# Kernel optimization log

Hardware: AMD Instinct MI355X
Metric: run time of the kernel (lower is better)

Reference implementation:

```python
import jax, jax.numpy as jnp
import numpy as np

D_MODEL = 1024
NUM_HEADS = 16
D_K = D_MODEL // NUM_HEADS


def setup_inputs() -> dict:
    key = jax.random.key(0)
    ks = jax.random.split(key, 11)
    B, S = 4, 2048
    s = 1.0 / np.sqrt(D_MODEL)
    return {
        "query": jax.random.normal(ks[0], (B, S, D_MODEL), jnp.float32),
        "key": jax.random.normal(ks[1], (B, S, D_MODEL), jnp.float32),
        "value": jax.random.normal(ks[2], (B, S, D_MODEL), jnp.float32),
        "Wq": jax.random.normal(ks[3], (D_MODEL, D_MODEL), jnp.float32) * s,
        "bq": jnp.zeros((D_MODEL,), jnp.float32),
        "Wk": jax.random.normal(ks[4], (D_MODEL, D_MODEL), jnp.float32) * s,
        "bk": jnp.zeros((D_MODEL,), jnp.float32),
        "Wv": jax.random.normal(ks[5], (D_MODEL, D_MODEL), jnp.float32) * s,
        "bv": jnp.zeros((D_MODEL,), jnp.float32),
        "Wo": jax.random.normal(ks[6], (D_MODEL, D_MODEL), jnp.float32) * s,
        "bo": jnp.zeros((D_MODEL,), jnp.float32),
    }


def reference(query, key, value, Wq, bq, Wk, bk, Wv, bv, Wo, bo):
    B, Sq, _ = query.shape
    Sk = key.shape[1]
    # linear projections (torch Linear: x @ W.T + b)
    q = query @ Wq.T + bq
    k = key @ Wk.T + bk
    v = value @ Wv.T + bv
    # [B, H, S, d_k]
    q = q.reshape(B, Sq, NUM_HEADS, D_K).transpose(0, 2, 1, 3)
    k = k.reshape(B, Sk, NUM_HEADS, D_K).transpose(0, 2, 1, 3)
    v = v.reshape(B, Sk, NUM_HEADS, D_K).transpose(0, 2, 1, 3)
    scores = jnp.einsum("bhqd,bhkd->bhqk", q, k) / jnp.sqrt(jnp.float32(D_K)).astype(q.dtype)
    attn = jax.nn.softmax(scores, axis=-1)
    out = jnp.einsum("bhqk,bhkd->bhqd", attn, v)
    out = out.transpose(0, 2, 1, 3).reshape(B, Sq, D_MODEL)
    return out @ Wo.T + bo
```

## Files before the change

kernel.cpp:

```cpp
#include <hip/hip_runtime.h>
#include <hip/hip_bf16.h>
#include <cstdint>
#include <cstddef>

typedef __attribute__((ext_vector_type(8))) short bf16x8;
typedef __attribute__((ext_vector_type(4))) short bf16x4;
typedef __attribute__((ext_vector_type(4))) float f32x4;
typedef __attribute__((ext_vector_type(2))) unsigned int u32x2;
typedef __attribute__((ext_vector_type(4))) unsigned int u32x4;

#define NH 16
#define DK 64
#define SEQ 2048
#define DM 1024
#define QSCALE 0.18033688011112042f

__device__ __forceinline__ short f2bf(float f) {
    union { float f; unsigned u; } x; x.f = f;
    unsigned r = x.u + 0x7fffu + ((x.u >> 16) & 1u);
    return (short)(r >> 16);
}

__device__ __forceinline__ unsigned pk2(float a, float b) {
    union { float f; unsigned u; } x, y; x.f = a; y.f = b;
    return __builtin_amdgcn_perm(y.u + 0x8000u, x.u + 0x8000u, 0x07060302u);
}

__device__ __forceinline__ unsigned cvtpk(float a, float b) {
    unsigned r;
    asm("v_cvt_pk_bf16_f32 %0, %1, %2" : "=v"(r) : "v"(a), "v"(b));
    return r;
}

__device__ __forceinline__ void plswap32(unsigned& a, unsigned& b) {
    asm("v_permlane32_swap_b32 %0, %1" : "+v"(a), "+v"(b));
}

__device__ __forceinline__ void glds16(const short* g, short* l) {
    __builtin_amdgcn_global_load_lds((const __attribute__((address_space(1))) unsigned int*)g,
                                     (__attribute__((address_space(3))) unsigned int*)l, 16, 0, 0);
}

__global__ __launch_bounds__(256)
void cvt_all(const float* __restrict__ xq, const float* __restrict__ xk, const float* __restrict__ xv,
             const float* __restrict__ Wq, const float* __restrict__ Wk,
             const float* __restrict__ Wv, const float* __restrict__ Wo,
             short* __restrict__ xb0, short* __restrict__ xb1, short* __restrict__ xb2,
             short* __restrict__ Wb)
{
    const int bid = blockIdx.x;
    const float* src;
    short* dst;
    float sc = 1.0f;
    int i;
    if (bid < 12288) {
        int z = bid >> 12;
        src = (z == 0) ? xq : (z == 1) ? xk : xv;
        dst = (z == 0) ? xb0 : (z == 1) ? xb1 : xb2;
        i = (bid & 4095) * 2048 + threadIdx.x * 8;
    } else {
        int wb = bid - 12288;
        int z = wb >> 9;
        src = (z == 0) ? Wq : (z == 1) ? Wk : (z == 2) ? Wv : Wo;
        dst = Wb + (size_t)z * DM * DM;
        sc = (z == 0) ? QSCALE : 1.0f;
        i = (wb & 511) * 2048 + threadIdx.x * 8;
    }
    float4 a = *(const float4*)&src[i];
    float4 b = *(const float4*)&src[i + 4];
    bf16x8 o = { f2bf(a.x * sc), f2bf(a.y * sc), f2bf(a.z * sc), f2bf(a.w * sc),
                 f2bf(b.x * sc), f2bf(b.y * sc), f2bf(b.z * sc), f2bf(b.w * sc) };
    *(bf16x8*)&dst[i] = o;
}

__global__ __launch_bounds__(256)
void cvt_x(const float* __restrict__ src, short* __restrict__ dst)
{
    int i = (blockIdx.x * 256 + threadIdx.x) * 8;
    float4 a = *(const float4*)&src[i];
    float4 b = *(const float4*)&src[i + 4];
    bf16x8 o = { f2bf(a.x), f2bf(a.y), f2bf(a.z), f2bf(a.w),
                 f2bf(b.x), f2bf(b.y), f2bf(b.z), f2bf(b.w) };
    *(bf16x8*)&dst[i] = o;
}

__global__ __launch_bounds__(256)
void cvt_w(const float* __restrict__ Wq, const float* __restrict__ Wk,
           const float* __restrict__ Wv, const float* __restrict__ Wo,
           short* __restrict__ dst)
{
    int z = blockIdx.y;
    const float* s = (z == 0) ? Wq : (z == 1) ? Wk : (z == 2) ? Wv : Wo;
    float sc = (z == 0) ? QSCALE : 1.0f;
    int i = (blockIdx.x * 256 + threadIdx.x) * 8;
    float4 a = *(const float4*)&s[i];
    float4 b = *(const float4*)&s[i + 4];
    bf16x8 o = { f2bf(a.x * sc), f2bf(a.y * sc), f2bf(a.z * sc), f2bf(a.w * sc),
                 f2bf(b.x * sc), f2bf(b.y * sc), f2bf(b.z * sc), f2bf(b.w * sc) };
    *(bf16x8*)&dst[(size_t)z * DM * DM + i] = o;
}

#define GEMM_CORE(P0, OFF0, P1, OFF1)                                                      \
    __shared__ short As[128 * 32];                                                         \
    __shared__ short Bs[128 * 32];                                                         \
    f32x4 acc[4][4] = {};                                                                  \
    const int t = threadIdx.x;                                                             \
    const int lane = t & 63;                                                               \
    const int w = t >> 6;                                                                  \
    const int wm = (w >> 1) * 64, wn = (w & 1) * 64;                                       \
    const int l15 = lane & 15, quad = lane >> 4;                                           \
    const int g0 = t, g1 = 256 + t;                                                        \
    const int r0 = g0 >> 2, r1 = g1 >> 2;                                                  \
    const int c0 = ((g0 & 3) ^ ((r0 >> 1) & 3)) * 8;                                       \
    const int c1 = ((g1 & 3) ^ ((r1 >> 1) & 3)) * 8;                                       \
    for (int k0 = 0; k0 < DM; k0 += 32) {                                                  \
        glds16(&P0[(size_t)(OFF0 + r0) * DM + k0 + c0], &As[g0 * 8]);                      \
        glds16(&P0[(size_t)(OFF0 + r1) * DM + k0 + c1], &As[g1 * 8]);                      \
        glds16(&P1[(size_t)(OFF1 + r0) * DM + k0 + c0], &Bs[g0 * 8]);                      \
        glds16(&P1[(size_t)(OFF1 + r1) * DM + k0 + c1], &Bs[g1 * 8]);                      \
        __syncthreads();                                                                   \
        bf16x8 a[4], b[4];                                                                 \
        _Pragma("unroll")                                                                  \
        for (int i = 0; i < 4; i++) {                                                      \
            int row = wm + i * 16 + l15;                                                   \
            a[i] = *(bf16x8*)&As[row * 32 + (quad ^ ((row >> 1) & 3)) * 8];                \
        }                                                                                  \
        _Pragma("unroll")                                                                  \
        for (int j = 0; j < 4; j++) {                                                      \
            int row = wn + j * 16 + l15;                                                   \
            b[j] = *(bf16x8*)&Bs[row * 32 + (quad ^ ((row >> 1) & 3)) * 8];                \
        }                                                                                  \
        _Pragma("unroll")                                                                  \
        for (int i = 0; i < 4; i++)                                                        \
            _Pragma("unroll")                                                              \
            for (int j = 0; j < 4; j++)                                                    \
                acc[i][j] = __builtin_amdgcn_mfma_f32_16x16x32_bf16(a[i], b[j], acc[i][j], 0, 0, 0); \
        __syncthreads();                                                                   \
    }

__global__ __launch_bounds__(256)
void gemm_qkv(const short* __restrict__ x0, const short* __restrict__ x1, const short* __restrict__ x2,
              const short* __restrict__ Wball,
              const float* __restrict__ bq, const float* __restrict__ bk, const float* __restrict__ bv,
              short* __restrict__ qws, short* __restrict__ kws, short* __restrict__ vws,
              int zoff)
{
    const int z = blockIdx.z + zoff;
    const short* X = (z == 0) ? x0 : (z == 1) ? x1 : x2;
    const short* W = Wball + (size_t)z * DM * DM;
    const float* bias = (z == 0) ? bq : (z == 1) ? bk : bv;
    const float bscale = (z == 0) ? QSCALE : 1.0f;

    const int tn = blockIdx.x * 128;
    const int tm = blockIdx.y * 128;
    const int vm = (z == 2);

    const short* P0 = vm ? X : W;   const int OFF0 = vm ? tm : tn;
    const short* P1 = vm ? W : X;   const int OFF1 = vm ? tn : tm;
    GEMM_CORE(P0, OFF0, P1, OFF1)

    if (vm) {
#pragma unroll
        for (int j = 0; j < 4; j++) {
            int n = tn + wn + j * 16 + l15;
            float bn = bias[n];
            int h = n >> 6, d = n & 63;
#pragma unroll
            for (int i = 0; i < 4; i++) {
                int m0 = tm + wm + i * 16 + quad * 4;
                int bb = m0 >> 11, s0 = m0 & (SEQ - 1);
                int g = (s0 >> 2) & 7;
                int gp = (g & 4) | ((g & 1) << 1) | ((g >> 1) & 1);
                int sp = (s0 & ~31) | (gp << 2);
                u32x2 u = { pk2(acc[i][j][0] + bn, acc[i][j][1] + bn),
                            pk2(acc[i][j][2] + bn, acc[i][j][3] + bn) };
                *(u32x2*)&vws[((size_t)((bb * NH + h) * 64 + d)) * SEQ + sp] = u;
            }
        }
    } else {
        short* dst = (z == 0) ? qws : kws;
#pragma unroll
        for (int i = 0; i < 4; i++) {
            int n0 = tn + wm + i * 16 + quad * 4;
            float4 b4 = *(const float4*)&bias[n0];
            int h = n0 >> 6, d0 = n0 & 63;
#pragma unroll
            for (int j = 0; j < 4; j++) {
                int m = tm + wn + j * 16 + l15;
                int bb = m >> 11, s = m & (SEQ - 1);
                u32x2 u = { pk2(acc[i][j][0] + b4.x * bscale, acc[i][j][1] + b4.y * bscale),
                            pk2(acc[i][j][2] + b4.z * bscale, acc[i][j][3] + b4.w * bscale) };
                *(u32x2*)&dst[((((size_t)(bb * NH + h)) * SEQ + s) << 6) + d0] = u;
            }
        }
    }
}

__global__ __launch_bounds__(256)
void out_proj(const short* __restrict__ A, const short* __restrict__ W,
              const float* __restrict__ bias, float* __restrict__ out)
{
    const int tn = blockIdx.x * 128;
    const int tm = blockIdx.y * 128;
    GEMM_CORE(A, tm, W, tn)

#pragma unroll
    for (int j = 0; j < 4; j++) {
        int n = tn + wn + j * 16 + l15;
        float bn = bias[n];
#pragma unroll
        for (int i = 0; i < 4; i++)
#pragma unroll
            for (int r = 0; r < 4; r++) {
                int m = tm + wm + i * 16 + quad * 4 + r;
                out[(size_t)m * DM + n] = acc[i][j][r] + bn;
            }
    }
}

__global__ __launch_bounds__(256, 4)
void attn(const short* __restrict__ Q, const short* __restrict__ K, const short* __restrict__ V,
          short* __restrict__ O)
{
    const int qt = blockIdx.x;
    const int bh = blockIdx.y;
    const int b = bh >> 4, h = bh & 15;
    const size_t base = (size_t)bh * SEQ * DK;
    const size_t vbase = (size_t)bh * DK * SEQ;

    const int t = threadIdx.x;
    const int lane = t & 63;
    const int w = t >> 6;
    const int l15 = lane & 15, quad = lane >> 4;
    const int l7 = l15 & 7;

    __shared__ short Kt[2][64 * 64];
    __shared__ short Vt[2][80 * 64];

    {
        int buf = t >> 7;
        int row = 64 + ((t >> 3) & 15);
        short val = (row == 64) ? (short)0x3F80 : (short)0;
        bf16x8 fill = { val, val, val, val, val, val, val, val };
        *(bf16x8*)&Vt[buf][row * 64 + (t & 7) * 8] = fill;
    }

    const int sr = t >> 3, su = t & 7;
    const int swz = (su ^ (sr & 7)) * 8;
    const short* kp0 = &K[base + (size_t)sr * DK + swz];
    const short* vp0 = &V[vbase + (size_t)sr * SEQ + swz];

    glds16(kp0,               &Kt[0][sr * 64 + su * 8]);
    glds16(kp0 + 32 * DK,     &Kt[0][(32 + sr) * 64 + su * 8]);
    glds16(vp0,               &Vt[0][sr * 64 + su * 8]);
    glds16(vp0 + 32 * SEQ,    &Vt[0][(32 + sr) * 64 + su * 8]);

    bf16x8 qb[2][2];
    const int qrow0 = qt * 128 + w * 32;
#pragma unroll
    for (int nq = 0; nq < 2; nq++)
#pragma unroll
        for (int kd = 0; kd < 2; kd++)
            qb[nq][kd] = *(const bf16x8*)&Q[base + (size_t)(qrow0 + nq * 16 + l15) * DK + kd * 32 + quad * 8];

    f32x4 oT[5][2] = {};

    for (int kt = 0; kt < SEQ / 64; kt++) {
        __syncthreads();
        const int cur = kt & 1;
        if (kt < SEQ / 64 - 1) {
            const int nxt = cur ^ 1;
            const int kb = (kt + 1) * 64;
            glds16(kp0 + (size_t)kb * DK,        &Kt[nxt][sr * 64 + su * 8]);
            glds16(kp0 + (size_t)(kb + 32) * DK, &Kt[nxt][(32 + sr) * 64 + su * 8]);
            glds16(vp0 + kb,                     &Vt[nxt][sr * 64 + su * 8]);
            glds16(vp0 + kb + 32 * SEQ,          &Vt[nxt][(32 + sr) * 64 + su * 8]);
        }

#pragma unroll
        for (int half = 0; half < 2; half++) {
            f32x4 st[2][2] = {};
#pragma unroll
            for (int kd = 0; kd < 2; kd++) {
#pragma unroll
                for (int m2 = 0; m2 < 2; m2++) {
                    const int mf = half * 2 + m2;
                    bf16x8 ka = *(bf16x8*)&Kt[cur][(mf * 16 + l15) * 64 + ((kd * 4 + quad) ^ l7) * 8];
#pragma unroll
                    for (int nq = 0; nq < 2; nq++)
                        st[m2][nq] = __builtin_amdgcn_mfma_f32_16x16x32_bf16(ka, qb[nq][kd], st[m2][nq], 0, 0, 0);
                }
            }

            bf16x8 pb[2];
#pragma unroll
            for (int nq = 0; nq < 2; nq++) {
#pragma unroll
                for (int m2 = 0; m2 < 2; m2++)
#pragma unroll
                    for (int r = 0; r < 4; r++)
                        st[m2][nq][r] = __builtin_amdgcn_exp2f(st[m2][nq][r]);
                unsigned W0 = cvtpk(st[0][nq][0], st[0][nq][1]);
                unsigned W1 = cvtpk(st[0][nq][2], st[0][nq][3]);
                unsigned W2 = cvtpk(st[1][nq][0], st[1][nq][1]);
                unsigned W3 = cvtpk(st[1][nq][2], st[1][nq][3]);
                plswap32(W0, W2);
                plswap32(W1, W3);
                u32x4 uu = { W0, W1, W2, W3 };
                pb[nq] = *(bf16x8*)&uu;
            }

#pragma unroll
            for (int mfd = 0; mfd < 5; mfd++) {
                bf16x8 va = *(bf16x8*)&Vt[cur][(mfd * 16 + l15) * 64 + ((half * 4 + quad) ^ l7) * 8];
#pragma unroll
                for (int nq = 0; nq < 2; nq++)
                    oT[mfd][nq] = __builtin_amdgcn_mfma_f32_16x16x32_bf16(va, pb[nq], oT[mfd][nq], 0, 0, 0);
            }
        }
    }

#pragma unroll
    for (int nq = 0; nq < 2; nq++) {
        float lsum = __shfl(oT[4][nq][0], l15);
        float inv = 1.0f / lsum;
        int s = qrow0 + nq * 16 + l15;
#pragma unroll
        for (int mfd = 0; mfd < 4; mfd++) {
            u32x2 u = { cvtpk(oT[mfd][nq][0] * inv, oT[mfd][nq][1] * inv),
                        cvtpk(oT[mfd][nq][2] * inv, oT[mfd][nq][3] * inv) };
            *(u32x2*)&O[((size_t)(b * SEQ + s)) * DM + h * 64 + mfd * 16 + quad * 4] = u;
        }
    }
}

extern "C" void kernel_launch(void* const* d_in, const int* in_sizes, int n_in,
                              void* d_out, int out_size, void* d_ws, size_t ws_size,
                              hipStream_t stream)
{
    const float* q_in = (const float*)d_in[0];
    const float* k_in = (const float*)d_in[1];
    const float* v_in = (const float*)d_in[2];
    const float* Wq = (const float*)d_in[3];
    const float* bq = (const float*)d_in[4];
    const float* Wk = (const float*)d_in[5];
    const float* bk = (const float*)d_in[6];
    const float* Wv = (const float*)d_in[7];
    const float* bv = (const float*)d_in[8];
    const float* Wo = (const float*)d_in[9];
    const float* bo = (const float*)d_in[10];
    float* out = (float*)d_out;

    char* ws = (char*)d_ws;
    const size_t MB = (size_t)1024 * 1024;
    short* qws = (short*)d_out;
    short* kws = (short*)d_out + (size_t)8 * MB;
    const size_t NW = (size_t)DM * DM;

    if (ws_size >= 88 * MB) {
        short* xb0 = (short*)(ws);
        short* xb1 = (short*)(ws + 16 * MB);
        short* xb2 = (short*)(ws + 32 * MB);
        short* vws = (short*)(ws + 48 * MB);
        short* ows = (short*)(ws + 64 * MB);
        short* Wb  = (short*)(ws + 80 * MB);

        cvt_all<<<dim3(14336), 256, 0, stream>>>(q_in, k_in, v_in, Wq, Wk, Wv, Wo, xb0, xb1, xb2, Wb);
        gemm_qkv<<<dim3(8, 64, 3), 256, 0, stream>>>(xb0, xb1, xb2, Wb, bq, bk, bv, qws, kws, vws, 0);
        attn<<<dim3(16, 64), 256, 0, stream>>>(qws, kws, vws, ows);
        out_proj<<<dim3(8, 64), 256, 0, stream>>>(ows, Wb + 3 * NW, bo, out);
    } else {
        short* xb  = (short*)(ws);
        short* vws = (short*)(ws + 16 * MB);
        short* ows = (short*)(ws + 32 * MB);
        short* Wb  = (short*)(ws + 48 * MB);
        const int xblocks = (4 * SEQ * DM) / 2048;

        cvt_w<<<dim3((int)(NW / 2048), 4), 256, 0, stream>>>(Wq, Wk, Wv, Wo, Wb);
        cvt_x<<<dim3(xblocks), 256, 0, stream>>>(q_in, xb);
        gemm_qkv<<<dim3(8, 64, 1), 256, 0, stream>>>(xb, xb, xb, Wb, bq, bk, bv, qws, kws, vws, 0);
        cvt_x<<<dim3(xblocks), 256, 0, stream>>>(k_in, xb);
        gemm_qkv<<<dim3(8, 64, 1), 256, 0, stream>>>(xb, xb, xb, Wb, bq, bk, bv, qws, kws, vws, 1);
        cvt_x<<<dim3(xblocks), 256, 0, stream>>>(v_in, xb);
        gemm_qkv<<<dim3(8, 64, 1), 256, 0, stream>>>(xb, xb, xb, Wb, bq, bk, bv, qws, kws, vws, 2);
        attn<<<dim3(16, 64), 256, 0, stream>>>(qws, kws, vws, ows);
        out_proj<<<dim3(8, 64), 256, 0, stream>>>(ows, Wb + 3 * NW, bo, out);
    }
}
```

Before: 345.8 us.

## Double attention query tile per block to reuse K/V tiles across more rows

```diff
diff --git a/kernel.cpp b/kernel.cpp
--- a/kernel.cpp
+++ b/kernel.cpp
@@ -218,7 +218,7 @@
     }
 }
 
-__global__ __launch_bounds__(256, 4)
+__global__ __launch_bounds__(256, 2)
 void attn(const short* __restrict__ Q, const short* __restrict__ K, const short* __restrict__ V,
           short* __restrict__ O)
 {
@@ -255,15 +255,15 @@
     glds16(vp0,               &Vt[0][sr * 64 + su * 8]);
     glds16(vp0 + 32 * SEQ,    &Vt[0][(32 + sr) * 64 + su * 8]);
 
-    bf16x8 qb[2][2];
-    const int qrow0 = qt * 128 + w * 32;
-#pragma unroll
-    for (int nq = 0; nq < 2; nq++)
+    bf16x8 qb[4][2];
+    const int qrow0 = qt * 256 + w * 64;
+#pragma unroll
+    for (int nq = 0; nq < 4; nq++)
 #pragma unroll
         for (int kd = 0; kd < 2; kd++)
             qb[nq][kd] = *(const bf16x8*)&Q[base + (size_t)(qrow0 + nq * 16 + l15) * DK + kd * 32 + quad * 8];
 
-    f32x4 oT[5][2] = {};
+    f32x4 oT[5][4] = {};
 
     for (int kt = 0; kt < SEQ / 64; kt++) {
         __syncthreads();
@@ -279,49 +279,56 @@
 
 #pragma unroll
         for (int half = 0; half < 2; half++) {
-            f32x4 st[2][2] = {};
-#pragma unroll
-            for (int kd = 0; kd < 2; kd++) {
-#pragma unroll
-                for (int m2 = 0; m2 < 2; m2++) {
-                    const int mf = half * 2 + m2;
-                    bf16x8 ka = *(bf16x8*)&Kt[cur][(mf * 16 + l15) * 64 + ((kd * 4 + quad) ^ l7) * 8];
-#pragma unroll
-                    for (int nq = 0; nq < 2; nq++)
-                        st[m2][nq] = __builtin_amdgcn_mfma_f32_16x16x32_bf16(ka, qb[nq][kd], st[m2][nq], 0, 0, 0);
+            bf16x8 ka[2][2];
+#pragma unroll
+            for (int m2 = 0; m2 < 2; m2++)
+#pragma unroll
+                for (int kd = 0; kd < 2; kd++)
+                    ka[m2][kd] = *(bf16x8*)&Kt[cur][((half * 2 + m2) * 16 + l15) * 64 + ((kd * 4 + quad) ^ l7) * 8];
+
+            bf16x8 pb[4];
+#pragma unroll
+            for (int np = 0; np < 2; np++) {
+                f32x4 st[2][2] = {};
+#pragma unroll
+                for (int kd = 0; kd < 2; kd++)
+#pragma unroll
+                    for (int m2 = 0; m2 < 2; m2++)
+#pragma unroll
+                        for (int n2 = 0; n2 < 2; n2++)
+                            st[m2][n2] = __builtin_amdgcn_mfma_f32_16x16x32_bf16(
+                                ka[m2][kd], qb[np * 2 + n2][kd], st[m2][n2], 0, 0, 0);
+
+#pragma unroll
+                for (int n2 = 0; n2 < 2; n2++) {
+#pragma unroll
+                    for (int m2 = 0; m2 < 2; m2++)
+#pragma unroll
+                        for (int r = 0; r < 4; r++)
+                            st[m2][n2][r] = __builtin_amdgcn_exp2f(st[m2][n2][r]);
+                    unsigned W0 = cvtpk(st[0][n2][0], st[0][n2][1]);
+                    unsigned W1 = cvtpk(st[0][n2][2], st[0][n2][3]);
+                    unsigned W2 = cvtpk(st[1][n2][0], st[1][n2][1]);
+                    unsigned W3 = cvtpk(st[1][n2][2], st[1][n2][3]);
+                    plswap32(W0, W2);
+                    plswap32(W1, W3);
+                    u32x4 uu = { W0, W1, W2, W3 };
+                    pb[np * 2 + n2] = *(bf16x8*)&uu;
                 }
-            }
-
-            bf16x8 pb[2];
-#pragma unroll
-            for (int nq = 0; nq < 2; nq++) {
-#pragma unroll
-                for (int m2 = 0; m2 < 2; m2++)
-#pragma unroll
-                    for (int r = 0; r < 4; r++)
-                        st[m2][nq][r] = __builtin_amdgcn_exp2f(st[m2][nq][r]);
-                unsigned W0 = cvtpk(st[0][nq][0], st[0][nq][1]);
-                unsigned W1 = cvtpk(st[0][nq][2], st[0][nq][3]);
-                unsigned W2 = cvtpk(st[1][nq][0], st[1][nq][1]);
-                unsigned W3 = cvtpk(st[1][nq][2], st[1][nq][3]);
-                plswap32(W0, W2);
-                plswap32(W1, W3);
-                u32x4 uu = { W0, W1, W2, W3 };
-                pb[nq] = *(bf16x8*)&uu;
             }
 
 #pragma unroll
             for (int mfd = 0; mfd < 5; mfd++) {
                 bf16x8 va = *(bf16x8*)&Vt[cur][(mfd * 16 + l15) * 64 + ((half * 4 + quad) ^ l7) * 8];
 #pragma unroll
-                for (int nq = 0; nq < 2; nq++)
+                for (int nq = 0; nq < 4; nq++)
                     oT[mfd][nq] = __builtin_amdgcn_mfma_f32_16x16x32_bf16(va, pb[nq], oT[mfd][nq], 0, 0, 0);
             }
         }
     }
 
 #pragma unroll
-    for (int nq = 0; nq < 2; nq++) {
+    for (int nq = 0; nq < 4; nq++) {
         float lsum = __shfl(oT[4][nq][0], l15);
         float inv = 1.0f / lsum;
         int s = qrow0 + nq * 16 + l15;
@@ -367,7 +374,7 @@
 
         cvt_all<<<dim3(14336), 256, 0, stream>>>(q_in, k_in, v_in, Wq, Wk, Wv, Wo, xb0, xb1, xb2, Wb);
         gemm_qkv<<<dim3(8, 64, 3), 256, 0, stream>>>(xb0, xb1, xb2, Wb, bq, bk, bv, qws, kws, vws, 0);
-        attn<<<dim3(16, 64), 256, 0, stream>>>(qws, kws, vws, ows);
+        attn<<<dim3(8, 64), 256, 0, stream>>>(qws, kws, vws, ows);
         out_proj<<<dim3(8, 64), 256, 0, stream>>>(ows, Wb + 3 * NW, bo, out);
     } else {
         short* xb  = (short*)(ws);
@@ -383,7 +390,7 @@
         gemm_qkv<<<dim3(8, 64, 1), 256, 0, stream>>>(xb, xb, xb, Wb, bq, bk, bv, qws, kws, vws, 1);
         cvt_x<<<dim3(xblocks), 256, 0, stream>>>(v_in, xb);
         gemm_qkv<<<dim3(8, 64, 1), 256, 0, stream>>>(xb, xb, xb, Wb, bq, bk, bv, qws, kws, vws, 2);
-        attn<<<dim3(16, 64), 256, 0, stream>>>(qws, kws, vws, ows);
+        attn<<<dim3(8, 64), 256, 0, stream>>>(qws, kws, vws, ows);
         out_proj<<<dim3(8, 64), 256, 0, stream>>>(ows, Wb + 3 * NW, bo, out);
     }
 }
```

Result: no change. 345.5 us (-0.1%).
